# Kernel tuning notes

Measured on AMD Instinct MI355X. Metric: run time of the kernel, lower is better.

## Reference

```python
import jax, jax.numpy as jnp
import numpy as np

B, N, E = 2, 50000, 400000
FIN, HID, OUT = 128, 128, 128
EPS = 1e-5  # BatchNorm1d default eps


def setup_inputs() -> dict:
    key = jax.random.key(0)
    ks = jax.random.split(key, 12)
    x = jax.random.normal(ks[0], (B, N, FIN), dtype=jnp.float32)
    row = jax.random.randint(ks[1], (E,), 0, N, dtype=jnp.int32)          # scatter dst
    col = jnp.concatenate([jnp.arange(N, dtype=jnp.int32),                # ensure deg>=1
                           jax.random.randint(ks[2], (E - N,), 0, N, dtype=jnp.int32)])
    edge_index = jnp.stack([row, col])                                    # [2, E]
    deg = jnp.zeros((N,), jnp.float32).at[col].add(1.0)                   # degree(col, N)
    dis = deg ** -0.5
    norm = (dis[row] * dis[col])[None, :, None]                           # [1, E, 1]
    W1 = jax.random.normal(ks[3], (HID, FIN), jnp.float32) / np.sqrt(FIN)
    b1 = jax.random.normal(ks[4], (HID,), jnp.float32) * 0.01
    g1 = jnp.ones((N,), jnp.float32)
    be1 = jnp.zeros((N,), jnp.float32)
    W2 = jax.random.normal(ks[5], (OUT, HID), jnp.float32) / np.sqrt(HID)
    b2 = jax.random.normal(ks[6], (OUT,), jnp.float32) * 0.01
    g2 = jnp.ones((N,), jnp.float32)
    be2 = jnp.zeros((N,), jnp.float32)
    return {"x": x, "edge_index": edge_index, "norm": norm,
            "W1": W1, "b1": b1, "g1": g1, "be1": be1,
            "W2": W2, "b2": b2, "g2": g2, "be2": be2}


def _gcn_layer(x, edge_index, norm, W, b, g, be):
    # Linear (dropout p=0 -> identity)
    h = jnp.einsum('bnf,of->bno', x, W) + b                 # [B, N, C]
    # BatchNorm1d(num_features=N): per-node stats over (batch, channel)
    mu = jnp.mean(h, axis=(0, 2), keepdims=True)            # [1, N, 1]
    var = jnp.var(h, axis=(0, 2), keepdims=True)            # biased, as torch
    y = g[None, :, None] * (h - mu) * jax.lax.rsqrt(var + EPS) + be[None, :, None]
    a = jax.nn.gelu(y, approximate=False)                   # torch GELU = exact erf
    # message passing: gather src nodes, scale by norm, scatter-add to dst
    msgs = a[:, edge_index[1], :] * norm                    # [B, E, C]
    return jnp.zeros_like(a).at[:, edge_index[0], :].add(msgs)


def reference(x, edge_index, norm, W1, b1, g1, be1, W2, b2, g2, be2):
    x = _gcn_layer(x, edge_index, norm, W1, b1, g1, be1)
    x = _gcn_layer(x, edge_index, norm, W2, b2, g2, be2)
    return x
```

## Files before the change

### kernel.cpp

```cpp
#include <hip/hip_runtime.h>
#include <math.h>

#define CC 128
#define TNODES 32
#define TPAD 132

typedef unsigned short u16;
typedef short bf16x8 __attribute__((ext_vector_type(8)));
typedef short bf16x4 __attribute__((ext_vector_type(4)));
typedef float f32x4 __attribute__((ext_vector_type(4)));

__device__ __forceinline__ u16 f2bf(float f) {
    union { float f; unsigned u; } v; v.f = f;
    unsigned u = v.u;
    return (u16)((u + 0x7FFFu + ((u >> 16) & 1u)) >> 16);
}
__device__ __forceinline__ float bf2f(unsigned hi16) {
    union { unsigned u; float f; } v; v.u = hi16 << 16; return v.f;
}

__device__ __forceinline__ float gelu_f(float y) {
    float xa = fabsf(y) * 0.70710678118654752f;
    float t  = __builtin_amdgcn_rcpf(fmaf(0.3275911f, xa, 1.0f));
    float p  = fmaf(1.061405429f, t, -1.453152027f);
    p = fmaf(p, t, 1.421413741f);
    p = fmaf(p, t, -0.284496736f);
    p = fmaf(p, t, 0.254829592f);
    p *= t;
    float e  = __expf(-xa * xa);
    float er = fmaf(-p, e, 1.0f);
    float s  = copysignf(er, y);
    return 0.5f * y * (1.0f + s);
}


__global__ __launch_bounds__(256) void k_zero_i32(int* __restrict__ p, int n) {
    int i = blockIdx.x * 256 + threadIdx.x;
    if (i < n) p[i] = 0;
}

__global__ __launch_bounds__(256) void k_hist(const int* __restrict__ row, int* __restrict__ cnt, int E) {
    int e = blockIdx.x * 256 + threadIdx.x;
    if (e < E) atomicAdd(&cnt[row[e]], 1);
}

__device__ __forceinline__ int wave_incl_scan(int v) {
    #pragma unroll
    for (int d = 1; d < 64; d <<= 1) {
        int t = __shfl_up(v, d);
        if ((threadIdx.x & 63) >= d) v += t;
    }
    return v;
}

__global__ __launch_bounds__(256) void k_scan_a(const int* __restrict__ cnt, int* __restrict__ bsum, int N) {
    int base = blockIdx.x * 1024 + threadIdx.x * 4;
    int s = 0;
    #pragma unroll
    for (int u = 0; u < 4; ++u) { int i = base + u; if (i < N) s += cnt[i]; }
    #pragma unroll
    for (int d = 32; d > 0; d >>= 1) s += __shfl_down(s, d);
    __shared__ int wsum[4];
    if ((threadIdx.x & 63) == 0) wsum[threadIdx.x >> 6] = s;
    __syncthreads();
    if (threadIdx.x == 0) bsum[blockIdx.x] = wsum[0] + wsum[1] + wsum[2] + wsum[3];
}

__global__ __launch_bounds__(64) void k_scan_b(const int* __restrict__ bsum, int* __restrict__ boff,
                                               int* __restrict__ off, int N, int nb) {
    int carry = 0;
    for (int base = 0; base < nb; base += 64) {
        int t = base + (int)threadIdx.x;
        int v = (t < nb) ? bsum[t] : 0;
        int incl = wave_incl_scan(v);
        if (t < nb) boff[t] = carry + incl - v;
        carry += __shfl(incl, 63);
    }
    if (threadIdx.x == 0) off[N] = carry;
}

__global__ __launch_bounds__(256) void k_scan_c(int* __restrict__ cnt, const int* __restrict__ boff,
                                                int* __restrict__ off, int N) {
    int t = threadIdx.x;
    int base = blockIdx.x * 1024 + t * 4;
    int v[4]; int s = 0;
    #pragma unroll
    for (int u = 0; u < 4; ++u) { int i = base + u; v[u] = (i < N) ? cnt[i] : 0; s += v[u]; }
    int incl = wave_incl_scan(s);
    __shared__ int wsum[4];
    int w = t >> 6, lane = t & 63;
    if (lane == 63) wsum[w] = incl;
    __syncthreads();
    int run = incl - s + boff[blockIdx.x];
    for (int ww = 0; ww < w; ++ww) run += wsum[ww];
    #pragma unroll
    for (int u = 0; u < 4; ++u) {
        int i = base + u;
        if (i < N) { off[i] = run; cnt[i] = 0; }
        run += v[u];
    }
}

__global__ __launch_bounds__(256) void k_fill(const int* __restrict__ row, const int* __restrict__ col,
                                              const float* __restrict__ nrm, const int* __restrict__ off,
                                              int* __restrict__ cur, int2* __restrict__ eg, int E) {
    int e = blockIdx.x * 256 + threadIdx.x;
    if (e < E) {
        int r = row[e];
        int p = off[r] + atomicAdd(&cur[r], 1);
        eg[p] = make_int2(col[e], __float_as_int(nrm[e]));
    }
}

__global__ __launch_bounds__(256) void k_wrepack(const float* __restrict__ W1, u16* __restrict__ Wp1,
                                                 const float* __restrict__ W2, u16* __restrict__ Wp2) {
    int i = blockIdx.x * 256 + threadIdx.x;
    const float* W = (i < CC * CC) ? W1 : W2;
    u16* Wp = (i < CC * CC) ? Wp1 : Wp2;
    int ii = (i < CC * CC) ? i : i - CC * CC;
    if (ii < CC * CC) {
        int j = ii & 7, l = (ii >> 3) & 63, s = (ii >> 9) & 3, t = ii >> 11;
        int r = 16 * t + (l & 15);
        int k = s * 32 + (l >> 4) * 8 + j;
        Wp[ii] = f2bf(W[r * CC + k]);
    }
}

template<int IN_BF16>
__global__ __launch_bounds__(256) void k_gemm_bn_gelu(
    const void* __restrict__ Xv, const u16* __restrict__ Wp,
    const float* __restrict__ bias, const float* __restrict__ gamma, const float* __restrict__ beta,
    u16* __restrict__ Out, int N)
{
    __shared__ u16 T[64][TPAD];
    __shared__ float rowS[64], rowQ[64], SCv[TNODES], SHv[TNODES];

    const int tid = threadIdx.x;
    const int w = tid >> 6;
    const int l = tid & 63;
    const int g = l >> 4;
    const int c = l & 15;
    const int n0 = blockIdx.x * TNODES;

    const int am = w * 16 + c;
    const int ab = am >> 5;
    const int an = n0 + (am & 31);
    const bool avalid = an < N;

    bf16x8 af[4];
    if (IN_BF16) {
        const u16* X = (const u16*)Xv;
        const u16* base = X + ((size_t)ab * N + an) * CC + g * 8;
        #pragma unroll
        for (int s = 0; s < 4; ++s) {
            bf16x8 v = {0, 0, 0, 0, 0, 0, 0, 0};
            if (avalid) v = *(const bf16x8*)(base + s * 32);
            af[s] = v;
        }
    } else {
        const float* X = (const float*)Xv;
        const float* base = X + ((size_t)ab * N + an) * CC + g * 8;
        #pragma unroll
        for (int s = 0; s < 4; ++s) {
            float4 lo = make_float4(0.f, 0.f, 0.f, 0.f), hi = lo;
            if (avalid) {
                lo = *(const float4*)(base + s * 32);
                hi = *(const float4*)(base + s * 32 + 4);
            }
            bf16x8 v;
            v[0] = (short)f2bf(lo.x); v[1] = (short)f2bf(lo.y);
            v[2] = (short)f2bf(lo.z); v[3] = (short)f2bf(lo.w);
            v[4] = (short)f2bf(hi.x); v[5] = (short)f2bf(hi.y);
            v[6] = (short)f2bf(hi.z); v[7] = (short)f2bf(hi.w);
            af[s] = v;
        }
    }

    f32x4 acc[8];
    #pragma unroll
    for (int t = 0; t < 8; ++t) acc[t] = (f32x4){0.f, 0.f, 0.f, 0.f};

    #pragma unroll
    for (int s = 0; s < 4; ++s) {
        bf16x8 bf[8];
        #pragma unroll
        for (int t = 0; t < 8; ++t)
            bf[t] = *(const bf16x8*)(Wp + (((size_t)(t * 4 + s) * 64) + l) * 8);
        #pragma unroll
        for (int t = 0; t < 8; ++t)
            acc[t] = __builtin_amdgcn_mfma_f32_16x16x32_bf16(af[s], bf[t], acc[t], 0, 0, 0);
    }

    float bb[8];
    #pragma unroll
    for (int t = 0; t < 8; ++t) bb[t] = bias[t * 16 + c];

    float rs[4] = {0.f, 0.f, 0.f, 0.f}, rq[4] = {0.f, 0.f, 0.f, 0.f};
    #pragma unroll
    for (int t = 0; t < 8; ++t)
        #pragma unroll
        for (int r = 0; r < 4; ++r) {
            float h = acc[t][r] + bb[t];
            acc[t][r] = h;
            rs[r] += h;
            rq[r] += h * h;
        }
    #pragma unroll
    for (int d = 1; d < 16; d <<= 1) {
        #pragma unroll
        for (int r = 0; r < 4; ++r) {
            rs[r] += __shfl_xor(rs[r], d);
            rq[r] += __shfl_xor(rq[r], d);
        }
    }
    if (c == 0) {
        #pragma unroll
        for (int r = 0; r < 4; ++r) {
            rowS[w * 16 + g * 4 + r] = rs[r];
            rowQ[w * 16 + g * 4 + r] = rq[r];
        }
    }
    __syncthreads();

    if (tid < TNODES) {
        float s = rowS[tid] + rowS[tid + 32];
        float q = rowQ[tid] + rowQ[tid + 32];
        float mean = s * (1.f / 256.f);
        float var  = q * (1.f / 256.f) - mean * mean;
        int node = n0 + tid;
        float gam = (node < N) ? gamma[node] : 1.f;
        float bet = (node < N) ? beta[node]  : 0.f;
        float sc = gam * rsqrtf(fmaxf(var, 0.f) + 1e-5f);
        SCv[tid] = sc;
        SHv[tid] = bet - mean * sc;
    }
    __syncthreads();

    #pragma unroll
    for (int r = 0; r < 4; ++r) {
        int dr = w * 16 + g * 4 + r;
        float sc = SCv[dr & 31], sh = SHv[dr & 31];
        #pragma unroll
        for (int t = 0; t < 8; ++t) {
            float y = acc[t][r] * sc + sh;
            T[dr][t * 16 + c] = f2bf(gelu_f(y));
        }
    }
    __syncthreads();

    #pragma unroll
    for (int q = 0; q < 4; ++q) {
        int chunk = q * 256 + tid;
        int rowi = chunk >> 4;
        int offc = (chunk & 15) * 8;
        int dn = rowi & 31, db = rowi >> 5;
        int node = n0 + dn;
        if (node < N) {
            bf16x4 lo = *(const bf16x4*)&T[rowi][offc];
            bf16x4 hi = *(const bf16x4*)&T[rowi][offc + 4];
            bf16x8 v;
            v[0] = lo[0]; v[1] = lo[1]; v[2] = lo[2]; v[3] = lo[3];
            v[4] = hi[0]; v[5] = hi[1]; v[6] = hi[2]; v[7] = hi[3];
            *(bf16x8*)(Out + ((size_t)db * N + node) * CC + offc) = v;
        }
    }
}

template<int OUT_F32>
__global__ __launch_bounds__(256) void k_aggregate(
    const u16* __restrict__ A, const int* __restrict__ off,
    const int2* __restrict__ eg, void* __restrict__ Outv, int N)
{
    int n = blockIdx.x * 4 + (threadIdx.x >> 6);
    if (n >= N) return;
    int l = threadIdx.x & 63;
    int b = l >> 5;
    int ch = (l & 31) * 4;
    const u16* Ab = A + (size_t)b * N * CC + ch;
    int s = off[n], e = off[n + 1];
    float a0 = 0.f, a1 = 0.f, a2 = 0.f, a3 = 0.f;
    int j = s;
    for (; j + 4 <= e; j += 4) {
        int2 e0 = eg[j], e1 = eg[j + 1], e2 = eg[j + 2], e3 = eg[j + 3];
        bf16x4 v0 = *(const bf16x4*)(Ab + (size_t)e0.x * CC);
        bf16x4 v1 = *(const bf16x4*)(Ab + (size_t)e1.x * CC);
        bf16x4 v2 = *(const bf16x4*)(Ab + (size_t)e2.x * CC);
        bf16x4 v3 = *(const bf16x4*)(Ab + (size_t)e3.x * CC);
        float w0 = __int_as_float(e0.y), w1 = __int_as_float(e1.y);
        float w2 = __int_as_float(e2.y), w3 = __int_as_float(e3.y);
        a0 = fmaf(w0, bf2f((u16)v0[0]), a0); a1 = fmaf(w0, bf2f((u16)v0[1]), a1);
        a2 = fmaf(w0, bf2f((u16)v0[2]), a2); a3 = fmaf(w0, bf2f((u16)v0[3]), a3);
        a0 = fmaf(w1, bf2f((u16)v1[0]), a0); a1 = fmaf(w1, bf2f((u16)v1[1]), a1);
        a2 = fmaf(w1, bf2f((u16)v1[2]), a2); a3 = fmaf(w1, bf2f((u16)v1[3]), a3);
        a0 = fmaf(w2, bf2f((u16)v2[0]), a0); a1 = fmaf(w2, bf2f((u16)v2[1]), a1);
        a2 = fmaf(w2, bf2f((u16)v2[2]), a2); a3 = fmaf(w2, bf2f((u16)v2[3]), a3);
        a0 = fmaf(w3, bf2f((u16)v3[0]), a0); a1 = fmaf(w3, bf2f((u16)v3[1]), a1);
        a2 = fmaf(w3, bf2f((u16)v3[2]), a2); a3 = fmaf(w3, bf2f((u16)v3[3]), a3);
    }
    for (; j < e; ++j) {
        int2 e0 = eg[j];
        float wt = __int_as_float(e0.y);
        bf16x4 v = *(const bf16x4*)(Ab + (size_t)e0.x * CC);
        a0 = fmaf(wt, bf2f((u16)v[0]), a0);
        a1 = fmaf(wt, bf2f((u16)v[1]), a1);
        a2 = fmaf(wt, bf2f((u16)v[2]), a2);
        a3 = fmaf(wt, bf2f((u16)v[3]), a3);
    }
    if (OUT_F32) {
        float* d = (float*)Outv + (size_t)b * N * CC + (size_t)n * CC + ch;
        d[0] = a0; d[1] = a1; d[2] = a2; d[3] = a3;
    } else {
        u16* d = (u16*)Outv + (size_t)b * N * CC + (size_t)n * CC + ch;
        bf16x4 v;
        v[0] = (short)f2bf(a0); v[1] = (short)f2bf(a1);
        v[2] = (short)f2bf(a2); v[3] = (short)f2bf(a3);
        *(bf16x4*)d = v;
    }
}


extern "C" void kernel_launch(void* const* d_in, const int* in_sizes, int n_in,
                              void* d_out, int out_size, void* d_ws, size_t ws_size,
                              hipStream_t stream)
{
    const float* x   = (const float*)d_in[0];
    const int*   ei  = (const int*)d_in[1];
    const float* nrm = (const float*)d_in[2];
    const float* W1  = (const float*)d_in[3];
    const float* b1  = (const float*)d_in[4];
    const float* g1  = (const float*)d_in[5];
    const float* be1 = (const float*)d_in[6];
    const float* W2  = (const float*)d_in[7];
    const float* b2  = (const float*)d_in[8];
    const float* g2  = (const float*)d_in[9];
    const float* be2 = (const float*)d_in[10];

    const int N = in_sizes[5];
    const int E = in_sizes[2];
    const int* row = ei;
    const int* col = ei + E;
    const int nb = (N + 1023) / 1024;

    auto al = [](size_t v) { return (v + 255) & ~(size_t)255; };
    char* p = (char*)d_ws;
    int* off    = (int*)p;   p += al((size_t)(N + 1) * 4);
    int* cur    = (int*)p;   p += al((size_t)N * 4);
    int2* eg    = (int2*)p;  p += al((size_t)E * 8);
    int* bsum   = (int*)p;   p += al((size_t)nb * 4);
    int* boff   = (int*)p;   p += al((size_t)nb * 4);
    u16* Wp1    = (u16*)p;   p += al((size_t)CC * CC * 2);
    u16* Wp2    = (u16*)p;   p += al((size_t)CC * CC * 2);
    u16* bufA   = (u16*)p;   p += al((size_t)2 * N * CC * 2);
    u16* bufB   = (u16*)p;   p += al((size_t)2 * N * CC * 2);

    k_zero_i32<<<(N + 255) / 256, 256, 0, stream>>>(cur, N);
    k_hist<<<(E + 255) / 256, 256, 0, stream>>>(row, cur, E);
    k_scan_a<<<nb, 256, 0, stream>>>(cur, bsum, N);
    k_scan_b<<<1, 64, 0, stream>>>(bsum, boff, off, N, nb);
    k_scan_c<<<nb, 256, 0, stream>>>(cur, boff, off, N);
    k_fill<<<(E + 255) / 256, 256, 0, stream>>>(row, col, nrm, off, cur, eg, E);

    k_wrepack<<<(2 * CC * CC + 255) / 256, 256, 0, stream>>>(W1, Wp1, W2, Wp2);

    const int gb = (N + TNODES - 1) / TNODES;
    const int ga = (N + 3) / 4;
    k_gemm_bn_gelu<0><<<gb, 256, 0, stream>>>(x, Wp1, b1, g1, be1, bufA, N);
    k_aggregate<0><<<ga, 256, 0, stream>>>(bufA, off, eg, bufB, N);
    k_gemm_bn_gelu<1><<<gb, 256, 0, stream>>>(bufB, Wp2, b2, g2, be2, bufA, N);
    k_aggregate<1><<<ga, 256, 0, stream>>>(bufA, off, eg, (float*)d_out, N);
}
```

Before: 177.7 us.

## Make GEMM tile per-wave with in-register BN stats; widen aggregate gathers

The GEMM+BatchNorm+GELU kernel now gives each wave 8 nodes across both batches, so per-node statistics are reduced fully with wave shuffles. This drops the shared-memory row-sum arrays and two block barriers, and the LDS staging tile becomes per-wave. The aggregation kernel now loads 16-byte bf16x8 rows per lane and splits edges across two half-waves, combining them with a cross-half shuffle. This halves the load instructions per edge and increases memory-level parallelism, at the cost of predicated dummy loads on odd edge counts and idle lanes during the store.

```diff
diff --git a/kernel.cpp b/kernel.cpp
--- a/kernel.cpp
+++ b/kernel.cpp
@@ -2,7 +2,6 @@
 #include <math.h>
 
 #define CC 128
-#define TNODES 32
 #define TPAD 132
 
 typedef unsigned short u16;
@@ -132,41 +131,33 @@
     const float* __restrict__ bias, const float* __restrict__ gamma, const float* __restrict__ beta,
     u16* __restrict__ Out, int N)
 {
-    __shared__ u16 T[64][TPAD];
-    __shared__ float rowS[64], rowQ[64], SCv[TNODES], SHv[TNODES];
+    __shared__ u16 T[4][16][TPAD];
 
     const int tid = threadIdx.x;
     const int w = tid >> 6;
     const int l = tid & 63;
     const int g = l >> 4;
     const int c = l & 15;
-    const int n0 = blockIdx.x * TNODES;
-
-    const int am = w * 16 + c;
-    const int ab = am >> 5;
-    const int an = n0 + (am & 31);
-    const bool avalid = an < N;
+    const int n8 = blockIdx.x * 32 + w * 8;
+    const bool valid = n8 < N;
+    const int nbase = valid ? n8 : 0;
+
+    const int ab = c >> 3;
+    const int an = nbase + (c & 7);
 
     bf16x8 af[4];
     if (IN_BF16) {
         const u16* X = (const u16*)Xv;
         const u16* base = X + ((size_t)ab * N + an) * CC + g * 8;
         #pragma unroll
-        for (int s = 0; s < 4; ++s) {
-            bf16x8 v = {0, 0, 0, 0, 0, 0, 0, 0};
-            if (avalid) v = *(const bf16x8*)(base + s * 32);
-            af[s] = v;
-        }
+        for (int s = 0; s < 4; ++s) af[s] = *(const bf16x8*)(base + s * 32);
     } else {
         const float* X = (const float*)Xv;
         const float* base = X + ((size_t)ab * N + an) * CC + g * 8;
         #pragma unroll
         for (int s = 0; s < 4; ++s) {
-            float4 lo = make_float4(0.f, 0.f, 0.f, 0.f), hi = lo;
-            if (avalid) {
-                lo = *(const float4*)(base + s * 32);
-                hi = *(const float4*)(base + s * 32 + 4);
-            }
+            float4 lo = *(const float4*)(base + s * 32);
+            float4 hi = *(const float4*)(base + s * 32 + 4);
             bf16x8 v;
             v[0] = (short)f2bf(lo.x); v[1] = (short)f2bf(lo.y);
             v[2] = (short)f2bf(lo.z); v[3] = (short)f2bf(lo.w);
@@ -213,55 +204,51 @@
             rq[r] += __shfl_xor(rq[r], d);
         }
     }
-    if (c == 0) {
-        #pragma unroll
-        for (int r = 0; r < 4; ++r) {
-            rowS[w * 16 + g * 4 + r] = rs[r];
-            rowQ[w * 16 + g * 4 + r] = rq[r];
+    #pragma unroll
+    for (int r = 0; r < 4; ++r) {
+        rs[r] += __shfl_xor(rs[r], 32);
+        rq[r] += __shfl_xor(rq[r], 32);
+    }
+
+    float sc[4], sh[4];
+    #pragma unroll
+    for (int r = 0; r < 4; ++r) {
+        int p = (4 * g + r) & 7;
+        int node = nbase + p;
+        float mean = rs[r] * (1.f / 256.f);
+        float var  = rq[r] * (1.f / 256.f) - mean * mean;
+        float gam = gamma[node];
+        float bet = beta[node];
+        float s_ = gam * rsqrtf(fmaxf(var, 0.f) + 1e-5f);
+        sc[r] = s_;
+        sh[r] = bet - mean * s_;
+    }
+
+    #pragma unroll
+    for (int r = 0; r < 4; ++r) {
+        int row = 4 * g + r;
+        #pragma unroll
+        for (int t = 0; t < 8; ++t) {
+            float y = acc[t][r] * sc[r] + sh[r];
+            T[w][row][t * 16 + c] = f2bf(gelu_f(y));
         }
     }
     __syncthreads();
 
-    if (tid < TNODES) {
-        float s = rowS[tid] + rowS[tid + 32];
-        float q = rowQ[tid] + rowQ[tid + 32];
-        float mean = s * (1.f / 256.f);
-        float var  = q * (1.f / 256.f) - mean * mean;
-        int node = n0 + tid;
-        float gam = (node < N) ? gamma[node] : 1.f;
-        float bet = (node < N) ? beta[node]  : 0.f;
-        float sc = gam * rsqrtf(fmaxf(var, 0.f) + 1e-5f);
-        SCv[tid] = sc;
-        SHv[tid] = bet - mean * sc;
-    }
-    __syncthreads();
-
-    #pragma unroll
-    for (int r = 0; r < 4; ++r) {
-        int dr = w * 16 + g * 4 + r;
-        float sc = SCv[dr & 31], sh = SHv[dr & 31];
-        #pragma unroll
-        for (int t = 0; t < 8; ++t) {
-            float y = acc[t][r] * sc + sh;
-            T[dr][t * 16 + c] = f2bf(gelu_f(y));
-        }
-    }
-    __syncthreads();
-
-    #pragma unroll
-    for (int q = 0; q < 4; ++q) {
-        int chunk = q * 256 + tid;
-        int rowi = chunk >> 4;
-        int offc = (chunk & 15) * 8;
-        int dn = rowi & 31, db = rowi >> 5;
-        int node = n0 + dn;
-        if (node < N) {
-            bf16x4 lo = *(const bf16x4*)&T[rowi][offc];
-            bf16x4 hi = *(const bf16x4*)&T[rowi][offc + 4];
+    if (valid) {
+        #pragma unroll
+        for (int it = 0; it < 4; ++it) {
+            int chunk = it * 64 + l;
+            int rowi = chunk >> 4;
+            int offc = (chunk & 15) * 8;
+            int db = rowi >> 3;
+            int dn = n8 + (rowi & 7);
+            bf16x4 lo = *(const bf16x4*)&T[w][rowi][offc];
+            bf16x4 hi = *(const bf16x4*)&T[w][rowi][offc + 4];
             bf16x8 v;
             v[0] = lo[0]; v[1] = lo[1]; v[2] = lo[2]; v[3] = lo[3];
             v[4] = hi[0]; v[5] = hi[1]; v[6] = hi[2]; v[7] = hi[3];
-            *(bf16x8*)(Out + ((size_t)db * N + node) * CC + offc) = v;
+            *(bf16x8*)(Out + ((size_t)db * N + dn) * CC + offc) = v;
         }
     }
 }
@@ -274,47 +261,39 @@
     int n = blockIdx.x * 4 + (threadIdx.x >> 6);
     if (n >= N) return;
     int l = threadIdx.x & 63;
-    int b = l >> 5;
-    int ch = (l & 31) * 4;
-    const u16* Ab = A + (size_t)b * N * CC + ch;
+    int p = l >> 5;
+    int b = (l >> 4) & 1;
+    int ch0 = (l & 15) * 8;
+    const u16* Ab = A + (size_t)b * N * CC + ch0;
     int s = off[n], e = off[n + 1];
-    float a0 = 0.f, a1 = 0.f, a2 = 0.f, a3 = 0.f;
-    int j = s;
-    for (; j + 4 <= e; j += 4) {
-        int2 e0 = eg[j], e1 = eg[j + 1], e2 = eg[j + 2], e3 = eg[j + 3];
-        bf16x4 v0 = *(const bf16x4*)(Ab + (size_t)e0.x * CC);
-        bf16x4 v1 = *(const bf16x4*)(Ab + (size_t)e1.x * CC);
-        bf16x4 v2 = *(const bf16x4*)(Ab + (size_t)e2.x * CC);
-        bf16x4 v3 = *(const bf16x4*)(Ab + (size_t)e3.x * CC);
+    float a[8] = {0.f, 0.f, 0.f, 0.f, 0.f, 0.f, 0.f, 0.f};
+    for (int j = s; j < e; j += 4) {
+        int i0 = j + p, i1 = j + 2 + p;
+        int2 e0 = (i0 < e) ? eg[i0] : make_int2(0, 0);
+        int2 e1 = (i1 < e) ? eg[i1] : make_int2(0, 0);
+        bf16x8 v0 = *(const bf16x8*)(Ab + (size_t)e0.x * CC);
+        bf16x8 v1 = *(const bf16x8*)(Ab + (size_t)e1.x * CC);
         float w0 = __int_as_float(e0.y), w1 = __int_as_float(e1.y);
-        float w2 = __int_as_float(e2.y), w3 = __int_as_float(e3.y);
-        a0 = fmaf(w0, bf2f((u16)v0[0]), a0); a1 = fmaf(w0, bf2f((u16)v0[1]), a1);
-        a2 = fmaf(w0, bf2f((u16)v0[2]), a2); a3 = fmaf(w0, bf2f((u16)v0[3]), a3);
-        a0 = fmaf(w1, bf2f((u16)v1[0]), a0); a1 = fmaf(w1, bf2f((u16)v1[1]), a1);
-        a2 = fmaf(w1, bf2f((u16)v1[2]), a2); a3 = fmaf(w1, bf2f((u16)v1[3]), a3);
-        a0 = fmaf(w2, bf2f((u16)v2[0]), a0); a1 = fmaf(w2, bf2f((u16)v2[1]), a1);
-        a2 = fmaf(w2, bf2f((u16)v2[2]), a2); a3 = fmaf(w2, bf2f((u16)v2[3]), a3);
-        a0 = fmaf(w3, bf2f((u16)v3[0]), a0); a1 = fmaf(w3, bf2f((u16)v3[1]), a1);
-        a2 = fmaf(w3, bf2f((u16)v3[2]), a2); a3 = fmaf(w3, bf2f((u16)v3[3]), a3);
-    }
-    for (; j < e; ++j) {
-        int2 e0 = eg[j];
-        float wt = __int_as_float(e0.y);
-        bf16x4 v = *(const bf16x4*)(Ab + (size_t)e0.x * CC);
-        a0 = fmaf(wt, bf2f((u16)v[0]), a0);
-        a1 = fmaf(wt, bf2f((u16)v[1]), a1);
-        a2 = fmaf(wt, bf2f((u16)v[2]), a2);
-        a3 = fmaf(wt, bf2f((u16)v[3]), a3);
-    }
-    if (OUT_F32) {
-        float* d = (float*)Outv + (size_t)b * N * CC + (size_t)n * CC + ch;
-        d[0] = a0; d[1] = a1; d[2] = a2; d[3] = a3;
-    } else {
-        u16* d = (u16*)Outv + (size_t)b * N * CC + (size_t)n * CC + ch;
-        bf16x4 v;
-        v[0] = (short)f2bf(a0); v[1] = (short)f2bf(a1);
-        v[2] = (short)f2bf(a2); v[3] = (short)f2bf(a3);
-        *(bf16x4*)d = v;
+        #pragma unroll
+        for (int q = 0; q < 8; ++q) {
+            a[q] = fmaf(w0, bf2f((u16)v0[q]), a[q]);
+            a[q] = fmaf(w1, bf2f((u16)v1[q]), a[q]);
+        }
+    }
+    #pragma unroll
+    for (int q = 0; q < 8; ++q) a[q] += __shfl_xor(a[q], 32);
+    if (l < 32) {
+        if (OUT_F32) {
+            float* d = (float*)Outv + ((size_t)b * N + n) * CC + ch0;
+            *(float4*)&d[0] = make_float4(a[0], a[1], a[2], a[3]);
+            *(float4*)&d[4] = make_float4(a[4], a[5], a[6], a[7]);
+        } else {
+            u16* d = (u16*)Outv + ((size_t)b * N + n) * CC + ch0;
+            bf16x8 v;
+            #pragma unroll
+            for (int q = 0; q < 8; ++q) v[q] = (short)f2bf(a[q]);
+            *(bf16x8*)d = v;
+        }
     }
 }
 
@@ -362,7 +341,7 @@
 
     k_wrepack<<<(2 * CC * CC + 255) / 256, 256, 0, stream>>>(W1, Wp1, W2, Wp2);
 
-    const int gb = (N + TNODES - 1) / TNODES;
+    const int gb = (N + 31) / 32;
     const int ga = (N + 3) / 4;
     k_gemm_bn_gelu<0><<<gb, 256, 0, stream>>>(x, Wp1, b1, g1, be1, bufA, N);
     k_aggregate<0><<<ga, 256, 0, stream>>>(bufA, off, eg, bufB, N);
```

Measured after the change: 177.0 us. No clear change (-0.4%).
